# Kernel tuning notes

Measured on AMD Instinct MI355X. Metric: run time of the kernel, lower is better.

The kernel has to match this reference:

```python
import jax, jax.numpy as jnp
from jax import lax
import numpy as np

B = 262144   # batch of independent series
K = 64       # forecast horizon (init k)
D_IN = 200   # Non_AR_net input dim (Linear(200,100))
H = 100      # hidden width


def setup_inputs() -> dict:
    key = jax.random.key(0)
    ks = jax.random.split(key, 10)
    f32 = jnp.float32
    x = jax.random.normal(ks[0], (B, D_IN), f32)
    last_mu = jax.random.normal(ks[1], (B,), f32)
    # last_sigma is the variance state; keep it strictly positive
    last_sigma = jax.random.uniform(ks[2], (B,), f32) + 0.5
    # MLP params (Kaiming-ish scale)
    W1 = jax.random.normal(ks[3], (D_IN, H), f32) / np.float32(np.sqrt(D_IN))
    b1 = jnp.zeros((H,), f32)
    W2 = jax.random.normal(ks[4], (H, H), f32) / np.float32(np.sqrt(H))
    b2 = jnp.zeros((H,), f32)
    W3 = jax.random.normal(ks[5], (H, K), f32) / np.float32(np.sqrt(H))
    b3 = jnp.zeros((K,), f32)
    return {
        "x": x, "last_mu": last_mu, "last_sigma": last_sigma,
        "alpha_mu": jnp.asarray(0.1, f32), "alpha_sigma": jnp.asarray(0.1, f32),
        "beta_mu": jnp.asarray(0.9, f32), "beta_sigma": jnp.asarray(0.85, f32),
        "omega_mu": jnp.asarray(0.0, f32), "omega_sigma": jnp.asarray(0.05, f32),
        "nu": jnp.asarray(5.0, f32), "norm_strength": jnp.asarray(1.0, f32),
        "W1": W1, "b1": b1, "W2": W2, "b2": b2, "W3": W3, "b3": b3,
    }


def _mlp(x, W1, b1, W2, b2, W3, b3):
    h = jax.nn.relu(x @ W1 + b1)
    h = jax.nn.relu(h @ W2 + b2)
    return h @ W3 + b3  # [B, K]


def _ar_gas(deep_preds, last_mu, last_sigma, a_mu, a_s, b_mu, b_s, o_mu, o_s, nu, ns):
    """Student-t score-driven (GAS) k-step recurrence, vectorized over batch.
    deep_preds: [B, K]; state mu, sigma2: [B]."""
    w = 1.0 + 1.0 / nu

    def step(carry, y):  # y: [B]
        mu, s2 = carry
        e = y - mu
        denom = 1.0 + e * e / (nu * s2)
        mu_new = o_mu + ns * a_mu * (w * e / denom) + b_mu * mu
        s2_new = o_s + ns * a_s * (w * e * e / denom - s2) + b_s * s2
        return (mu_new, s2_new), (mu_new, s2_new)

    (_, _), (mus, s2s) = lax.scan(step, (last_mu, last_sigma), deep_preds.T)
    return mus.T, jnp.sqrt(s2s.T)  # [B, K] each


def reference(x, last_mu, last_sigma, alpha_mu, alpha_sigma, beta_mu, beta_sigma,
              omega_mu, omega_sigma, nu, norm_strength,
              W1, b1, W2, b2, W3, b3):
    deep_preds = _mlp(x, W1, b1, W2, b2, W3, b3)            # [B, K]
    dp = lax.stop_gradient(deep_preds)                       # .detach() in torch
    mu_pred, sigma_pred = _ar_gas(dp, last_mu, last_sigma,
                                  alpha_mu, alpha_sigma, beta_mu, beta_sigma,
                                  omega_mu, omega_sigma, nu, norm_strength)
    return deep_preds * sigma_pred + mu_pred                 # [B, K]
```

## Files before the change

### kernel.cpp

```cpp
#include <hip/hip_runtime.h>
#include <hip/hip_bf16.h>

typedef short v8s __attribute__((ext_vector_type(8)));
typedef float v4f __attribute__((ext_vector_type(4)));

#define THREADS 512
#define WAVES   8
#define BMROWS  128
#define W1F     0
#define W2F     49
#define W3F     77
#define W3B     33792
#define W2B     50176
#define SLAB_STRIDE 264
#define SLAB_SIZE   4224
#define LDS_TOTAL   78848

__device__ __forceinline__ unsigned short f2bf(float f) {
    union { __hip_bfloat16 h; unsigned short u; } c;
    c.h = __float2bfloat16(f);
    return c.u;
}
__device__ __forceinline__ unsigned pk2(float a, float b) {
    return (unsigned)f2bf(a) | ((unsigned)f2bf(b) << 16);
}
__device__ __forceinline__ v4f mfma16(v8s a, v8s b, v4f c) {
    return __builtin_amdgcn_mfma_f32_16x16x32_bf16(a, b, c, 0, 0, 0);
}
__device__ __forceinline__ v8s mkfrag(float4 a, float4 b) {
    union { unsigned u[4]; v8s s; } t;
    t.u[0] = pk2(a.x, a.y); t.u[1] = pk2(a.z, a.w);
    t.u[2] = pk2(b.x, b.y); t.u[3] = pk2(b.z, b.w);
    return t.s;
}
__device__ __forceinline__ void gload_lds16(const void* g, void* l) {
    __builtin_amdgcn_global_load_lds(
        (const __attribute__((address_space(1))) void*)g,
        (__attribute__((address_space(3))) void*)l, 16, 0, 0);
}

__global__ void prep_weights(const float* __restrict__ W1,
                             const float* __restrict__ W2,
                             const float* __restrict__ W3,
                             uint4* __restrict__ wf) {
    const int bid = blockIdx.x, l = threadIdx.x;
    const float* W; int K, N, KC, base, f;
    if (bid < 49)      { W = W1; K = 200; N = 100; KC = 7; base = W1F * 64; f = bid; }
    else if (bid < 77) { W = W2; K = 100; N = 100; KC = 4; base = W2F * 64; f = bid - 49; }
    else               { W = W3; K = 100; N = 64;  KC = 4; base = W3F * 64; f = bid - 77; }
    const int kc = f % KC;
    const int n  = (f / KC) * 16 + (l & 15);
    unsigned u[4];
    #pragma unroll
    for (int p = 0; p < 4; ++p) {
        const int k0 = kc * 32 + (l >> 4) * 8 + p * 2;
        const float a = (k0     < K && n < N) ? W[(size_t)k0 * N + n]       : 0.f;
        const float b = (k0 + 1 < K && n < N) ? W[(size_t)(k0 + 1) * N + n] : 0.f;
        u[p] = pk2(a, b);
    }
    wf[base + f * 64 + l] = make_uint4(u[0], u[1], u[2], u[3]);
}

__global__ __launch_bounds__(THREADS, 2)
void ar_gas_v17(const float* __restrict__ x,
                const float* __restrict__ last_mu,
                const float* __restrict__ last_sigma,
                const float* __restrict__ p_amu, const float* __restrict__ p_as,
                const float* __restrict__ p_bmu, const float* __restrict__ p_bs,
                const float* __restrict__ p_omu, const float* __restrict__ p_os,
                const float* __restrict__ p_nu,  const float* __restrict__ p_ns,
                const float* __restrict__ b1, const float* __restrict__ b2,
                const float* __restrict__ b3,
                const uint4* __restrict__ wf,
                float* __restrict__ out)
{
    extern __shared__ __align__(16) unsigned char L[];
    const int tid  = threadIdx.x;
    const int lane = tid & 63;
    const int wid  = tid >> 6;
    const int l15  = lane & 15;
    const int l4   = lane >> 4;
    const int blk  = blockIdx.x;

    const size_t gw = (size_t)blk * BMROWS + (size_t)wid * 16;
    const float* xp = x + (gw + l15) * 200;

    float4 xv[7][2];
    #pragma unroll
    for (int kc = 0; kc < 7; ++kc) {
        int kb = kc * 32 + l4 * 8;
        kb = (kb + 8 <= 200) ? kb : 168;
        xv[kc][0] = *(const float4*)(xp + kb);
        xv[kc][1] = *(const float4*)(xp + kb + 4);
    }
    const float mu_init = last_mu[gw + l15];
    const float s2_init = last_sigma[gw + l15];

    for (int s = wid; s < 77; s += WAVES) {
        unsigned char* dst = (s < 49) ? (L + s * 1024)
                                      : (L + W2B + (s - 49) * 1024);
        gload_lds16(wf + s * 64 + lane, dst);
    }
    __syncthreads();

#define FRAG_W1(f)  (*(const uint4*)(&L[(f) * 1024 + lane * 16]))
#define FRAG_W2(f)  (*(const uint4*)(&L[W2B + (f) * 1024 + lane * 16]))
#define FRAG_W3(f)  (*(const uint4*)(&L[W3B + (f) * 1024 + lane * 16]))

    const int sb      = wid * SLAB_SIZE;
    const int sb_epi  = sb + (l4 * 4) * SLAB_STRIDE + l15 * 2;
    const int sb_rd   = sb + l15 * SLAB_STRIDE + l4 * 16;
    const int sb_dpw  = sb + (l4 * 4) * SLAB_STRIDE + l15 * 4;
    const int sb_gas  = sb + l15 * SLAB_STRIDE;
    const int sb_st   = sb + l4 * SLAB_STRIDE + l15 * 16;

    v4f acc[7];
    #pragma unroll
    for (int nt = 0; nt < 7; ++nt) acc[nt] = (v4f){0.f, 0.f, 0.f, 0.f};

    #pragma unroll
    for (int kc = 0; kc < 7; ++kc) {
        uint4 bu[7];
        #pragma unroll
        for (int nt = 0; nt < 7; ++nt) bu[nt] = FRAG_W1(nt * 7 + kc);
        const v8s af = mkfrag(xv[kc][0], xv[kc][1]);
        #pragma unroll
        for (int nt = 0; nt < 7; ++nt)
            acc[nt] = mfma16(af, *(const v8s*)&bu[nt], acc[nt]);
    }

    __syncthreads();

    for (int s = wid; s < 16; s += WAVES)
        gload_lds16(wf + (W3F + s) * 64 + lane, L + W3B + s * 1024);

    {
        float bv[7];
        #pragma unroll
        for (int nt = 0; nt < 7; ++nt) {
            const int c = nt * 16 + l15;
            bv[nt] = (c < 100) ? b1[c] : 0.f;
        }
        #pragma unroll
        for (int nt = 0; nt < 7; ++nt)
            #pragma unroll
            for (int r = 0; r < 4; ++r) {
                const float v = fmaxf(acc[nt][r] + bv[nt], 0.f);
                *(unsigned short*)(&L[sb_epi + r * SLAB_STRIDE + nt * 32]) = f2bf(v);
            }
    }
    if (lane < 32)
        *(uint4*)(&L[sb + (lane >> 1) * SLAB_STRIDE + 224 + (lane & 1) * 16]) =
            make_uint4(0, 0, 0, 0);

    v4f acc2[7];
    #pragma unroll
    for (int nt = 0; nt < 7; ++nt) acc2[nt] = (v4f){0.f, 0.f, 0.f, 0.f};
    #pragma unroll
    for (int kc = 0; kc < 4; ++kc) {
        uint4 bu[7];
        #pragma unroll
        for (int nt = 0; nt < 7; ++nt) bu[nt] = FRAG_W2(nt * 4 + kc);
        uint4 t0 = *(const uint4*)(&L[sb_rd + kc * 64]);
        const v8s af = *(v8s*)&t0;
        #pragma unroll
        for (int nt = 0; nt < 7; ++nt)
            acc2[nt] = mfma16(af, *(const v8s*)&bu[nt], acc2[nt]);
    }
    {
        float bv[7];
        #pragma unroll
        for (int nt = 0; nt < 7; ++nt) {
            const int c = nt * 16 + l15;
            bv[nt] = (c < 100) ? b2[c] : 0.f;
        }
        #pragma unroll
        for (int nt = 0; nt < 7; ++nt)
            #pragma unroll
            for (int r = 0; r < 4; ++r) {
                const float v = fmaxf(acc2[nt][r] + bv[nt], 0.f);
                *(unsigned short*)(&L[sb_epi + r * SLAB_STRIDE + nt * 32]) = f2bf(v);
            }
    }

    __syncthreads();

    v4f acc3[4];
    #pragma unroll
    for (int nt = 0; nt < 4; ++nt) acc3[nt] = (v4f){0.f, 0.f, 0.f, 0.f};
    #pragma unroll
    for (int kc = 0; kc < 4; ++kc) {
        uint4 bu[4];
        #pragma unroll
        for (int nt = 0; nt < 4; ++nt) bu[nt] = FRAG_W3(nt * 4 + kc);
        uint4 t0 = *(const uint4*)(&L[sb_rd + kc * 64]);
        const v8s af = *(v8s*)&t0;
        #pragma unroll
        for (int nt = 0; nt < 4; ++nt)
            acc3[nt] = mfma16(af, *(const v8s*)&bu[nt], acc3[nt]);
    }
    {
        float bv[4];
        #pragma unroll
        for (int nt = 0; nt < 4; ++nt) bv[nt] = b3[nt * 16 + l15];
        #pragma unroll
        for (int nt = 0; nt < 4; ++nt)
            #pragma unroll
            for (int r = 0; r < 4; ++r)
                *(float*)(&L[sb_dpw + r * SLAB_STRIDE + nt * 64]) =
                    acc3[nt][r] + bv[nt];
    }

    if (lane < 16) {
        float mu = mu_init;
        float s2 = s2_init;
        const float anu = *p_nu,  ans = *p_ns;
        const float aMu = *p_amu, aSg = *p_as;
        const float bMu = *p_bmu, bSg = *p_bs;
        const float oMu = *p_omu, oSg = *p_os;
        const float w   = 1.f + __builtin_amdgcn_rcpf(anu);
        const float cmu = ans * aMu * w;
        const float cs  = ans * aSg * w;
        const float bs2 = bSg - ans * aSg;

#define GAS_STEP(Y, O)                                                  \
        {   const float e    = (Y) - mu;                                \
            const float nus2 = anu * s2;                                \
            const float den  = fmaf(e, e, nus2);                        \
            const float r0   = __builtin_amdgcn_rcpf(den);              \
            const float p    = e * nus2 * r0;                           \
            mu = fmaf(cmu, p, fmaf(bMu, mu, oMu));                      \
            s2 = fmaf(cs, e * p, fmaf(bs2, s2, oSg));                   \
            (O) = fmaf((Y), __builtin_amdgcn_sqrtf(s2), mu); }

        #pragma unroll
        for (int q = 0; q < 16; ++q) {
            float4 d = *(float4*)(&L[sb_gas + q * 16]);
            float o0, o1, o2, o3;
            GAS_STEP(d.x, o0); GAS_STEP(d.y, o1);
            GAS_STEP(d.z, o2); GAS_STEP(d.w, o3);
            *(float4*)(&L[sb_gas + q * 16]) = make_float4(o0, o1, o2, o3);
        }
#undef GAS_STEP
    }

    #pragma unroll
    for (int i = 0; i < 4; ++i) {
        float4 v = *(float4*)(&L[sb_st + i * (4 * SLAB_STRIDE)]);
        ((float4*)out)[gw * 16 + i * 64 + lane] = v;
    }
#undef FRAG_W1
#undef FRAG_W2
#undef FRAG_W3
}

extern "C" void kernel_launch(void* const* d_in, const int* in_sizes, int n_in,
                              void* d_out, int out_size, void* d_ws, size_t ws_size,
                              hipStream_t stream) {
    const float* x          = (const float*)d_in[0];
    const float* last_mu    = (const float*)d_in[1];
    const float* last_sigma = (const float*)d_in[2];
    const float* amu        = (const float*)d_in[3];
    const float* asig       = (const float*)d_in[4];
    const float* bmu        = (const float*)d_in[5];
    const float* bsig       = (const float*)d_in[6];
    const float* omu        = (const float*)d_in[7];
    const float* osig       = (const float*)d_in[8];
    const float* nu         = (const float*)d_in[9];
    const float* ns         = (const float*)d_in[10];
    const float* W1         = (const float*)d_in[11];
    const float* b1         = (const float*)d_in[12];
    const float* W2         = (const float*)d_in[13];
    const float* b2         = (const float*)d_in[14];
    const float* W3         = (const float*)d_in[15];
    const float* b3         = (const float*)d_in[16];
    float* out = (float*)d_out;

    uint4* wf = (uint4*)d_ws;
    prep_weights<<<93, 64, 0, stream>>>(W1, W2, W3, wf);

    hipFuncSetAttribute((const void*)ar_gas_v17,
                        hipFuncAttributeMaxDynamicSharedMemorySize, LDS_TOTAL);

    const int B = in_sizes[1];
    dim3 grid(B / BMROWS), block(THREADS);
    ar_gas_v17<<<grid, block, LDS_TOTAL, stream>>>(
        x, last_mu, last_sigma,
        amu, asig, bmu, bsig, omu, osig, nu, ns,
        b1, b2, b3, wf, out);
}
```

Before: 83.32 us.

## Process four row tiles per block with x prefetch and one-time weight staging

Each block now processes 512 rows as four sequential 16-row tiles per wave, loading all weight fragments into LDS once and prefetching the next tile's x rows into registers while the current tile computes. The mid-kernel barriers and the W3 reload into a reused LDS region are removed by giving weights and per-wave slabs separate LDS areas. This amortizes weight staging and hides global load latency, but raises LDS use to about 126KB, which likely drops residency to one block per CU and reduces latency hiding for the serial GAS recurrence.

Result: no change. 83.29 us (-0.0%).

```diff
diff --git a/kernel.cpp b/kernel.cpp
--- a/kernel.cpp
+++ b/kernel.cpp
@@ -6,15 +6,15 @@
 
 #define THREADS 512
 #define WAVES   8
-#define BMROWS  128
+#define NTILES  4
+#define BMROWS  512
 #define W1F     0
 #define W2F     49
 #define W3F     77
-#define W3B     33792
-#define W2B     50176
+#define SLABB   95232
 #define SLAB_STRIDE 264
 #define SLAB_SIZE   4224
-#define LDS_TOTAL   78848
+#define LDS_TOTAL   (SLABB + WAVES * SLAB_SIZE)
 
 __device__ __forceinline__ unsigned short f2bf(float f) {
     union { __hip_bfloat16 h; unsigned short u; } c;
@@ -62,7 +62,7 @@
 }
 
 __global__ __launch_bounds__(THREADS, 2)
-void ar_gas_v17(const float* __restrict__ x,
+void ar_gas_v18(const float* __restrict__ x,
                 const float* __restrict__ last_mu,
                 const float* __restrict__ last_sigma,
                 const float* __restrict__ p_amu, const float* __restrict__ p_as,
@@ -82,176 +82,179 @@
     const int l4   = lane >> 4;
     const int blk  = blockIdx.x;
 
-    const size_t gw = (size_t)blk * BMROWS + (size_t)wid * 16;
-    const float* xp = x + (gw + l15) * 200;
+    const float anu = *p_nu,  ans = *p_ns;
+    const float aMu = *p_amu, aSg = *p_as;
+    const float bMu = *p_bmu, bSg = *p_bs;
+    const float oMu = *p_omu, oSg = *p_os;
+    const float wS  = 1.f + __builtin_amdgcn_rcpf(anu);
+    const float cmu = ans * aMu * wS;
+    const float cs  = ans * aSg * wS;
+    const float bs2 = bSg - ans * aSg;
+
+#define XLOADT(dst, base_row, kk)                                       \
+    { int kb = (kk) * 32 + l4 * 8;                                      \
+      kb = (kb + 8 <= 200) ? kb : 168;     \
+      const float* p_ = x + ((base_row) + l15) * 200;                   \
+      dst[kk][0] = *(const float4*)(p_ + kb);                           \
+      dst[kk][1] = *(const float4*)(p_ + kb + 4); }
+
+    const size_t gw0 = (size_t)blk * BMROWS + (size_t)wid * 64;
 
     float4 xv[7][2];
     #pragma unroll
-    for (int kc = 0; kc < 7; ++kc) {
-        int kb = kc * 32 + l4 * 8;
-        kb = (kb + 8 <= 200) ? kb : 168;
-        xv[kc][0] = *(const float4*)(xp + kb);
-        xv[kc][1] = *(const float4*)(xp + kb + 4);
-    }
-    const float mu_init = last_mu[gw + l15];
-    const float s2_init = last_sigma[gw + l15];
-
-    for (int s = wid; s < 77; s += WAVES) {
-        unsigned char* dst = (s < 49) ? (L + s * 1024)
-                                      : (L + W2B + (s - 49) * 1024);
-        gload_lds16(wf + s * 64 + lane, dst);
-    }
+    for (int kc = 0; kc < 7; ++kc) XLOADT(xv, gw0, kc);
+
+    for (int s = wid; s < 93; s += WAVES)
+        gload_lds16(wf + s * 64 + lane, L + s * 1024);
     __syncthreads();
 
-#define FRAG_W1(f)  (*(const uint4*)(&L[(f) * 1024 + lane * 16]))
-#define FRAG_W2(f)  (*(const uint4*)(&L[W2B + (f) * 1024 + lane * 16]))
-#define FRAG_W3(f)  (*(const uint4*)(&L[W3B + (f) * 1024 + lane * 16]))
-
-    const int sb      = wid * SLAB_SIZE;
+#define FRAG_W1(f)  (*(const uint4*)(&L[(W1F + (f)) * 1024 + lane * 16]))
+#define FRAG_W2(f)  (*(const uint4*)(&L[(W2F + (f)) * 1024 + lane * 16]))
+#define FRAG_W3(f)  (*(const uint4*)(&L[(W3F + (f)) * 1024 + lane * 16]))
+
+    const int sb      = SLABB + wid * SLAB_SIZE;
     const int sb_epi  = sb + (l4 * 4) * SLAB_STRIDE + l15 * 2;
     const int sb_rd   = sb + l15 * SLAB_STRIDE + l4 * 16;
     const int sb_dpw  = sb + (l4 * 4) * SLAB_STRIDE + l15 * 4;
     const int sb_gas  = sb + l15 * SLAB_STRIDE;
     const int sb_st   = sb + l4 * SLAB_STRIDE + l15 * 16;
 
-    v4f acc[7];
-    #pragma unroll
-    for (int nt = 0; nt < 7; ++nt) acc[nt] = (v4f){0.f, 0.f, 0.f, 0.f};
-
-    #pragma unroll
-    for (int kc = 0; kc < 7; ++kc) {
-        uint4 bu[7];
-        #pragma unroll
-        for (int nt = 0; nt < 7; ++nt) bu[nt] = FRAG_W1(nt * 7 + kc);
-        const v8s af = mkfrag(xv[kc][0], xv[kc][1]);
-        #pragma unroll
-        for (int nt = 0; nt < 7; ++nt)
-            acc[nt] = mfma16(af, *(const v8s*)&bu[nt], acc[nt]);
-    }
-
-    __syncthreads();
-
-    for (int s = wid; s < 16; s += WAVES)
-        gload_lds16(wf + (W3F + s) * 64 + lane, L + W3B + s * 1024);
-
-    {
-        float bv[7];
-        #pragma unroll
-        for (int nt = 0; nt < 7; ++nt) {
-            const int c = nt * 16 + l15;
-            bv[nt] = (c < 100) ? b1[c] : 0.f;
-        }
-        #pragma unroll
-        for (int nt = 0; nt < 7; ++nt)
-            #pragma unroll
-            for (int r = 0; r < 4; ++r) {
-                const float v = fmaxf(acc[nt][r] + bv[nt], 0.f);
-                *(unsigned short*)(&L[sb_epi + r * SLAB_STRIDE + nt * 32]) = f2bf(v);
+    #pragma unroll 1
+    for (int t = 0; t < NTILES; ++t) {
+        const size_t gw = gw0 + t * 16;
+
+        const float mu_init = last_mu[gw + l15];
+        const float s2_init = last_sigma[gw + l15];
+
+        v4f acc[7];
+        #pragma unroll
+        for (int nt = 0; nt < 7; ++nt) acc[nt] = (v4f){0.f, 0.f, 0.f, 0.f};
+        #pragma unroll
+        for (int kc = 0; kc < 7; ++kc) {
+            uint4 bu[7];
+            #pragma unroll
+            for (int nt = 0; nt < 7; ++nt) bu[nt] = FRAG_W1(nt * 7 + kc);
+            const v8s af = mkfrag(xv[kc][0], xv[kc][1]);
+            #pragma unroll
+            for (int nt = 0; nt < 7; ++nt)
+                acc[nt] = mfma16(af, *(const v8s*)&bu[nt], acc[nt]);
+        }
+
+        if (t < NTILES - 1) {
+            #pragma unroll
+            for (int kc = 0; kc < 7; ++kc) XLOADT(xv, gw0 + (t + 1) * 16, kc);
+        }
+
+        {
+            float bv[7];
+            #pragma unroll
+            for (int nt = 0; nt < 7; ++nt) {
+                const int c = nt * 16 + l15;
+                bv[nt] = (c < 100) ? b1[c] : 0.f;
             }
-    }
-    if (lane < 32)
-        *(uint4*)(&L[sb + (lane >> 1) * SLAB_STRIDE + 224 + (lane & 1) * 16]) =
-            make_uint4(0, 0, 0, 0);
-
-    v4f acc2[7];
-    #pragma unroll
-    for (int nt = 0; nt < 7; ++nt) acc2[nt] = (v4f){0.f, 0.f, 0.f, 0.f};
-    #pragma unroll
-    for (int kc = 0; kc < 4; ++kc) {
-        uint4 bu[7];
-        #pragma unroll
-        for (int nt = 0; nt < 7; ++nt) bu[nt] = FRAG_W2(nt * 4 + kc);
-        uint4 t0 = *(const uint4*)(&L[sb_rd + kc * 64]);
-        const v8s af = *(v8s*)&t0;
-        #pragma unroll
-        for (int nt = 0; nt < 7; ++nt)
-            acc2[nt] = mfma16(af, *(const v8s*)&bu[nt], acc2[nt]);
-    }
-    {
-        float bv[7];
-        #pragma unroll
-        for (int nt = 0; nt < 7; ++nt) {
-            const int c = nt * 16 + l15;
-            bv[nt] = (c < 100) ? b2[c] : 0.f;
-        }
-        #pragma unroll
-        for (int nt = 0; nt < 7; ++nt)
-            #pragma unroll
-            for (int r = 0; r < 4; ++r) {
-                const float v = fmaxf(acc2[nt][r] + bv[nt], 0.f);
-                *(unsigned short*)(&L[sb_epi + r * SLAB_STRIDE + nt * 32]) = f2bf(v);
+            #pragma unroll
+            for (int nt = 0; nt < 7; ++nt)
+                #pragma unroll
+                for (int r = 0; r < 4; ++r) {
+                    const float v = fmaxf(acc[nt][r] + bv[nt], 0.f);
+                    *(unsigned short*)(&L[sb_epi + r * SLAB_STRIDE + nt * 32]) =
+                        f2bf(v);
+                }
+        }
+        if (lane < 32)
+            *(uint4*)(&L[sb + (lane >> 1) * SLAB_STRIDE + 224 + (lane & 1) * 16]) =
+                make_uint4(0, 0, 0, 0);
+
+        v4f acc2[7];
+        #pragma unroll
+        for (int nt = 0; nt < 7; ++nt) acc2[nt] = (v4f){0.f, 0.f, 0.f, 0.f};
+        #pragma unroll
+        for (int kc = 0; kc < 4; ++kc) {
+            uint4 bu[7];
+            #pragma unroll
+            for (int nt = 0; nt < 7; ++nt) bu[nt] = FRAG_W2(nt * 4 + kc);
+            uint4 t0 = *(const uint4*)(&L[sb_rd + kc * 64]);
+            const v8s af = *(v8s*)&t0;
+            #pragma unroll
+            for (int nt = 0; nt < 7; ++nt)
+                acc2[nt] = mfma16(af, *(const v8s*)&bu[nt], acc2[nt]);
+        }
+        {
+            float bv[7];
+            #pragma unroll
+            for (int nt = 0; nt < 7; ++nt) {
+                const int c = nt * 16 + l15;
+                bv[nt] = (c < 100) ? b2[c] : 0.f;
             }
-    }
-
-    __syncthreads();
-
-    v4f acc3[4];
-    #pragma unroll
-    for (int nt = 0; nt < 4; ++nt) acc3[nt] = (v4f){0.f, 0.f, 0.f, 0.f};
-    #pragma unroll
-    for (int kc = 0; kc < 4; ++kc) {
-        uint4 bu[4];
-        #pragma unroll
-        for (int nt = 0; nt < 4; ++nt) bu[nt] = FRAG_W3(nt * 4 + kc);
-        uint4 t0 = *(const uint4*)(&L[sb_rd + kc * 64]);
-        const v8s af = *(v8s*)&t0;
-        #pragma unroll
-        for (int nt = 0; nt < 4; ++nt)
-            acc3[nt] = mfma16(af, *(const v8s*)&bu[nt], acc3[nt]);
-    }
-    {
-        float bv[4];
-        #pragma unroll
-        for (int nt = 0; nt < 4; ++nt) bv[nt] = b3[nt * 16 + l15];
-        #pragma unroll
-        for (int nt = 0; nt < 4; ++nt)
-            #pragma unroll
-            for (int r = 0; r < 4; ++r)
-                *(float*)(&L[sb_dpw + r * SLAB_STRIDE + nt * 64]) =
-                    acc3[nt][r] + bv[nt];
-    }
-
-    if (lane < 16) {
-        float mu = mu_init;
-        float s2 = s2_init;
-        const float anu = *p_nu,  ans = *p_ns;
-        const float aMu = *p_amu, aSg = *p_as;
-        const float bMu = *p_bmu, bSg = *p_bs;
-        const float oMu = *p_omu, oSg = *p_os;
-        const float w   = 1.f + __builtin_amdgcn_rcpf(anu);
-        const float cmu = ans * aMu * w;
-        const float cs  = ans * aSg * w;
-        const float bs2 = bSg - ans * aSg;
-
+            #pragma unroll
+            for (int nt = 0; nt < 7; ++nt)
+                #pragma unroll
+                for (int r = 0; r < 4; ++r) {
+                    const float v = fmaxf(acc2[nt][r] + bv[nt], 0.f);
+                    *(unsigned short*)(&L[sb_epi + r * SLAB_STRIDE + nt * 32]) =
+                        f2bf(v);
+                }
+        }
+
+        v4f acc3[4];
+        #pragma unroll
+        for (int nt = 0; nt < 4; ++nt) acc3[nt] = (v4f){0.f, 0.f, 0.f, 0.f};
+        #pragma unroll
+        for (int kc = 0; kc < 4; ++kc) {
+            uint4 bu[4];
+            #pragma unroll
+            for (int nt = 0; nt < 4; ++nt) bu[nt] = FRAG_W3(nt * 4 + kc);
+            uint4 t0 = *(const uint4*)(&L[sb_rd + kc * 64]);
+            const v8s af = *(v8s*)&t0;
+            #pragma unroll
+            for (int nt = 0; nt < 4; ++nt)
+                acc3[nt] = mfma16(af, *(const v8s*)&bu[nt], acc3[nt]);
+        }
+        {
+            float bv[4];
+            #pragma unroll
+            for (int nt = 0; nt < 4; ++nt) bv[nt] = b3[nt * 16 + l15];
+            #pragma unroll
+            for (int nt = 0; nt < 4; ++nt)
+                #pragma unroll
+                for (int r = 0; r < 4; ++r)
+                    *(float*)(&L[sb_dpw + r * SLAB_STRIDE + nt * 64]) =
+                        acc3[nt][r] + bv[nt];
+        }
+
+        if (lane < 16) {
+            float mu = mu_init;
+            float s2 = s2_init;
 #define GAS_STEP(Y, O)                                                  \
-        {   const float e    = (Y) - mu;                                \
-            const float nus2 = anu * s2;                                \
-            const float den  = fmaf(e, e, nus2);                        \
-            const float r0   = __builtin_amdgcn_rcpf(den);              \
-            const float p    = e * nus2 * r0;                           \
-            mu = fmaf(cmu, p, fmaf(bMu, mu, oMu));                      \
-            s2 = fmaf(cs, e * p, fmaf(bs2, s2, oSg));                   \
-            (O) = fmaf((Y), __builtin_amdgcn_sqrtf(s2), mu); }
-
-        #pragma unroll
-        for (int q = 0; q < 16; ++q) {
-            float4 d = *(float4*)(&L[sb_gas + q * 16]);
-            float o0, o1, o2, o3;
-            GAS_STEP(d.x, o0); GAS_STEP(d.y, o1);
-            GAS_STEP(d.z, o2); GAS_STEP(d.w, o3);
-            *(float4*)(&L[sb_gas + q * 16]) = make_float4(o0, o1, o2, o3);
-        }
+            {   const float e    = (Y) - mu;                            \
+                const float nus2 = anu * s2;                            \
+                const float den  = fmaf(e, e, nus2);                    \
+                const float r0   = __builtin_amdgcn_rcpf(den);          \
+                const float p    = e * nus2 * r0;                       \
+                mu = fmaf(cmu, p, fmaf(bMu, mu, oMu));                  \
+                s2 = fmaf(cs, e * p, fmaf(bs2, s2, oSg));               \
+                (O) = fmaf((Y), __builtin_amdgcn_sqrtf(s2), mu); }
+            #pragma unroll
+            for (int q = 0; q < 16; ++q) {
+                float4 d = *(float4*)(&L[sb_gas + q * 16]);
+                float o0, o1, o2, o3;
+                GAS_STEP(d.x, o0); GAS_STEP(d.y, o1);
+                GAS_STEP(d.z, o2); GAS_STEP(d.w, o3);
+                *(float4*)(&L[sb_gas + q * 16]) = make_float4(o0, o1, o2, o3);
+            }
 #undef GAS_STEP
-    }
-
-    #pragma unroll
-    for (int i = 0; i < 4; ++i) {
-        float4 v = *(float4*)(&L[sb_st + i * (4 * SLAB_STRIDE)]);
-        ((float4*)out)[gw * 16 + i * 64 + lane] = v;
+        }
+
+        #pragma unroll
+        for (int i = 0; i < 4; ++i) {
+            float4 v = *(float4*)(&L[sb_st + i * (4 * SLAB_STRIDE)]);
+            ((float4*)out)[gw * 16 + i * 64 + lane] = v;
+        }
     }
 #undef FRAG_W1
 #undef FRAG_W2
 #undef FRAG_W3
+#undef XLOADT
 }
 
 extern "C" void kernel_launch(void* const* d_in, const int* in_sizes, int n_in,
@@ -279,12 +282,12 @@
     uint4* wf = (uint4*)d_ws;
     prep_weights<<<93, 64, 0, stream>>>(W1, W2, W3, wf);
 
-    hipFuncSetAttribute((const void*)ar_gas_v17,
+    hipFuncSetAttribute((const void*)ar_gas_v18,
                         hipFuncAttributeMaxDynamicSharedMemorySize, LDS_TOTAL);
 
     const int B = in_sizes[1];
     dim3 grid(B / BMROWS), block(THREADS);
-    ar_gas_v17<<<grid, block, LDS_TOTAL, stream>>>(
+    ar_gas_v18<<<grid, block, LDS_TOTAL, stream>>>(
         x, last_mu, last_sigma,
         amu, asig, bmu, bsig, omu, osig, nu, ns,
         b1, b2, b3, wf, out);
```
